# Optimization experiments

Measured on AMD Instinct MI355X. Metric: run time of the kernel, lower is better.

## Reference

```python
import jax, jax.numpy as jnp
import numpy as np

B, N, S, K = 8, 4096, 1024, 128   # clouds, pts/cloud, fps samples (ratio=0.25), max neighbors
R = 0.2                            # radius
DIN = 3                            # point feature dim


def setup_inputs() -> dict:
    key = jax.random.key(0)
    ks = jax.random.split(key, 8)
    x = jax.random.normal(ks[0], (B * N, DIN), dtype=jnp.float32)
    pos = jax.random.uniform(ks[1], (B * N, 3), dtype=jnp.float32)
    batch = jnp.repeat(jnp.arange(B, dtype=jnp.int32), N)
    def lin(k, fi, fo):
        return jax.random.normal(k, (fi, fo), dtype=jnp.float32) / np.float32(np.sqrt(fi))
    W1 = lin(ks[2], DIN + 3, 64); b1 = jnp.zeros((64,), jnp.float32)
    W2 = lin(ks[3], 64, 64);      b2 = jnp.zeros((64,), jnp.float32)
    W3 = lin(ks[4], 64, 128);     b3 = jnp.zeros((128,), jnp.float32)
    return {"x": x, "pos": pos, "W1": W1, "b1": b1, "W2": W2, "b2": b2,
            "W3": W3, "b3": b3, "batch": batch}


def _fps(pos3):
    """Farthest point sampling per cloud. pos3: [B,N,3] -> idx [B,S] (start at point 0)."""
    d0 = jnp.sum((pos3 - pos3[:, :1]) ** 2, axis=-1)  # [B,N]
    def step(min_d, _):
        nxt = jnp.argmax(min_d, axis=1).astype(jnp.int32)             # [B]
        p = jnp.take_along_axis(pos3, nxt[:, None, None], axis=1)      # [B,1,3]
        d = jnp.sum((pos3 - p) ** 2, axis=-1)
        return jnp.minimum(min_d, d), nxt
    _, idxs = jax.lax.scan(step, d0, None, length=S - 1)               # [S-1,B]
    first = jnp.zeros((B, 1), jnp.int32)
    return jnp.concatenate([first, idxs.T], axis=1)                    # [B,S]


def reference(x, pos, W1, b1, W2, b2, W3, b3, batch):
    x3 = x.reshape(B, N, DIN)
    pos3 = pos.reshape(B, N, 3)
    batch2 = batch.reshape(B, N)

    idx = _fps(pos3)                                                   # [B,S]
    q = jnp.take_along_axis(pos3, idx[:, :, None], axis=1)             # [B,S,3]

    # radius ball query, capped at K nearest within R (deterministic variant of torch radius)
    d2 = jnp.sum((q[:, :, None, :] - pos3[:, None, :, :]) ** 2, -1)    # [B,S,N]
    masked = jnp.where(d2 <= R * R, d2, jnp.inf)
    negd, nbr = jax.lax.top_k(-masked, K)                              # [B,S,K]
    valid = jnp.isfinite(negd)                                         # [B,S,K]

    gather = jax.vmap(lambda a, i: a[i])                                # per-cloud fancy gather
    xj = gather(x3, nbr)                                               # [B,S,K,DIN]
    pj = gather(pos3, nbr)                                             # [B,S,K,3]
    rel = pj - q[:, :, None, :]
    feat = jnp.concatenate([xj, rel], axis=-1)                         # [B,S,K,6]

    h = jax.nn.relu(feat @ W1 + b1)
    h = jax.nn.relu(h @ W2 + b2)
    h = h @ W3 + b3                                                    # plain last layer

    h = jnp.where(valid[..., None], h, -jnp.inf)
    out = jnp.max(h, axis=2)                                           # max aggregation [B,S,128]
    out = jnp.where(jnp.any(valid, axis=2)[..., None], out, 0.0)

    x_out = out.reshape(B * S, -1)
    pos_out = q.reshape(B * S, 3)
    batch_out = jnp.take_along_axis(batch2, idx, axis=1).reshape(B * S)
    return x_out, pos_out, batch_out
```

## Files before the change

### kernel.cpp

```cpp
#include <hip/hip_runtime.h>
#include <hip/hip_fp16.h>

#define BB    8
#define NPTS  4096
#define SS    1024
#define KK    128
#define CAP   512
#define NW    248
#define TPB   256
#define PPT   16

typedef _Float16 half8 __attribute__((ext_vector_type(8)));
typedef float    f32x4 __attribute__((ext_vector_type(4)));


struct __align__(16) FpsSm {
    float4 Pl[NPTS];
    unsigned long long wkey[2][4];
};
struct __align__(16) WkSm {
    float cd2[4][CAP];
    int   cidx[4][CAP];
    int   nbrL[4][KK];
    _Float16 W2t[64 * 64];
    _Float16 W3t[128 * 64];
    _Float16 h2buf[4][32 * 64];
    float csh[64];
    float cpart[4][128];
    float b2s[64];
    float b3s[128];
    unsigned tick;
};
union __align__(16) SMem {
    FpsSm f;
    WkSm  w;
    char  pad[84 * 1024];
};

__device__ __forceinline__ void st_rel(unsigned* p, unsigned v) {
    __hip_atomic_store(p, v, __ATOMIC_RELEASE, __HIP_MEMORY_SCOPE_AGENT);
}
__device__ __forceinline__ unsigned ld_acq(unsigned* p) {
    return __hip_atomic_load(p, __ATOMIC_ACQUIRE, __HIP_MEMORY_SCOPE_AGENT);
}

#define DPP_FMAX(CTRL)                                                                  \
    {                                                                                   \
        unsigned o = (unsigned)__builtin_amdgcn_update_dpp(                             \
            (int)__float_as_uint(m), (int)__float_as_uint(m), CTRL, 0xF, 0xF, false);   \
        m = fmaxf(m, __uint_as_float(o));                                               \
    }

__global__ __launch_bounds__(TPB) void fused_kernel(const float* __restrict__ pos,
                                                    const int* __restrict__ batch,
                                                    const float* __restrict__ x,
                                                    const float* __restrict__ W1,
                                                    const float* __restrict__ b1,
                                                    const float* __restrict__ W2,
                                                    const float* __restrict__ b2,
                                                    const float* __restrict__ W3,
                                                    const float* __restrict__ b3,
                                                    float* __restrict__ E,
                                                    float* __restrict__ pos_out,
                                                    float* __restrict__ batch_out,
                                                    float* __restrict__ xout,
                                                    unsigned* __restrict__ sync) {
    __shared__ SMem sm;
    int t = threadIdx.x, w = t >> 6, l = t & 63;

    if (blockIdx.x < BB) {
        __builtin_amdgcn_s_setprio(3);
        int b = blockIdx.x;
        const float* P = pos + (size_t)b * NPTS * 3;

        for (int i = t; i < NPTS; i += TPB) {
            sm.f.Pl[i] = make_float4(P[i * 3 + 0], P[i * 3 + 1], P[i * 3 + 2], 0.f);
        }
        float bval = (float)batch[(size_t)b * NPTS];
        for (int i = t; i < SS; i += TPB) batch_out[b * SS + i] = bval;

        float px[PPT], py[PPT], pz[PPT], md[PPT];
        int base = t * PPT;
#pragma unroll
        for (int j = 0; j < PPT; j++) {
            px[j] = P[(base + j) * 3 + 0];
            py[j] = P[(base + j) * 3 + 1];
            pz[j] = P[(base + j) * 3 + 2];
        }
        float c0x = P[0], c0y = P[1], c0z = P[2];
        float lm = -1.f;
#pragma unroll
        for (int j = 0; j < PPT; j++) {
            float dx = __fsub_rn(px[j], c0x);
            float dy = __fsub_rn(py[j], c0y);
            float dz = __fsub_rn(pz[j], c0z);
            md[j] = __fadd_rn(__fadd_rn(__fmul_rn(dx, dx), __fmul_rn(dy, dy)), __fmul_rn(dz, dz));
            lm = fmaxf(lm, md[j]);
        }
        if (t == 0) {
            float* qp = pos_out + (size_t)(b * SS) * 3;
            qp[0] = c0x; qp[1] = c0y; qp[2] = c0z;
        }
        __syncthreads();

        for (int s = 1; s < SS; s++) {
            int jsel = 0x7FFFFFFF;
#pragma unroll
            for (int j = PPT - 1; j >= 0; j--)
                if (md[j] == lm) jsel = base + j;

            float m = lm;
            DPP_FMAX(0x111)
            DPP_FMAX(0x112)
            DPP_FMAX(0x114)
            DPP_FMAX(0x118)
            DPP_FMAX(0x142)
            DPP_FMAX(0x143)
            float wm = __uint_as_float((unsigned)__builtin_amdgcn_readlane(__float_as_uint(m), 63));

            unsigned long long mask = __ballot(lm == wm);
            int L = __ffsll((long long)mask) - 1;
            int si = __builtin_amdgcn_readlane(jsel, L);

            if (l == 0)
                sm.f.wkey[s & 1][w] = (((unsigned long long)__float_as_uint(wm)) << 32) | (~(unsigned)si);
            __syncthreads();

            const unsigned long long* wk = sm.f.wkey[s & 1];
            unsigned long long g0 = wk[0] > wk[1] ? wk[0] : wk[1];
            unsigned long long g1 = wk[2] > wk[3] ? wk[2] : wk[3];
            unsigned long long g = g0 > g1 ? g0 : g1;
            int gi = (int)(~(unsigned)g);

            float4 c = sm.f.Pl[gi];
            if (t == 0) {
                float* qp = pos_out + (size_t)(b * SS + s) * 3;
                qp[0] = c.x; qp[1] = c.y; qp[2] = c.z;
                if ((s & 63) == 63) st_rel(&sync[b * 32], (unsigned)(s + 1));
            }
#pragma unroll
            for (int j = 0; j < PPT; j++) {
                float dx = __fsub_rn(px[j], c.x);
                float dy = __fsub_rn(py[j], c.y);
                float dz = __fsub_rn(pz[j], c.z);
                float d2 = __fadd_rn(__fadd_rn(__fmul_rn(dx, dx), __fmul_rn(dy, dy)), __fmul_rn(dz, dz));
                md[j] = fminf(md[j], d2);
                lm = (j == 0) ? fmaxf(-1.f, md[0]) : fmaxf(lm, md[j]);
            }
        }
        return;
    }

    int wid = blockIdx.x - BB;
    unsigned* ectr = &sync[256];
    unsigned* qctr = &sync[260];

    for (int id = wid * TPB + t; id < 32768 * 64; id += NW * TPB) {
        int c = id & 63;
        int n = id >> 6;
        float x0 = x[n * 3 + 0], x1 = x[n * 3 + 1], x2 = x[n * 3 + 2];
        float p0 = pos[n * 3 + 0], p1 = pos[n * 3 + 1], p2 = pos[n * 3 + 2];
        float v = x0 * W1[0 * 64 + c] + x1 * W1[1 * 64 + c] + x2 * W1[2 * 64 + c]
                + p0 * W1[3 * 64 + c] + p1 * W1[4 * 64 + c] + p2 * W1[5 * 64 + c];
        E[(size_t)n * 64 + c] = v;
    }
    if (l == 0) __hip_atomic_fetch_add(ectr, 1u, __ATOMIC_RELEASE, __HIP_MEMORY_SCOPE_AGENT);

    for (int i = t; i < 64 * 64; i += TPB) {
        int n = i >> 6, k = i & 63;
        sm.w.W2t[(n << 6) | (k ^ ((n & 7) << 3))] = (_Float16)W2[k * 64 + n];
    }
    for (int i = t; i < 128 * 64; i += TPB) {
        int n = i >> 6, k = i & 63;
        sm.w.W3t[(n << 6) | (k ^ ((n & 7) << 3))] = (_Float16)W3[k * 128 + n];
    }
    if (t < 64) sm.w.b2s[t] = b2[t];
    if (t < 128) sm.w.b3s[t] = b3[t];

    if (t == 0) {
        while (ld_acq(ectr) < NW * 4u) __builtin_amdgcn_s_sleep(16);
    }
    __syncthreads();

    int lhi = l >> 4, llo = l & 15;

    while (true) {
        if (t == 0) {
            unsigned k = __hip_atomic_fetch_add(qctr, 1u, __ATOMIC_RELAXED, __HIP_MEMORY_SCOPE_AGENT);
            sm.w.tick = k;
        }
        __syncthreads();
        unsigned k = sm.w.tick;
        if (k >= 2048u) break;
        int posi = (int)(k >> 3);
        int cb   = (int)(k & 7u);
        int q0g = cb * SS + posi * 4;
        unsigned need = (unsigned)(posi * 4 + 4);
        if (t == 0) {
            while (ld_acq(&sync[cb * 32]) < need) __builtin_amdgcn_s_sleep(16);
        }
        __syncthreads();

        {
            int qi = q0g + w;
            int bBase = cb * NPTS;
            const float* P = pos + (size_t)bBase * 3;
            float qx = pos_out[qi * 3 + 0], qy = pos_out[qi * 3 + 1], qz = pos_out[qi * 3 + 2];

            int total = 0;
            for (int n0 = 0; n0 < NPTS; n0 += 64) {
                int n = n0 + l;
                float xx = P[n * 3 + 0], yy = P[n * 3 + 1], zz = P[n * 3 + 2];
                float dx = __fsub_rn(qx, xx);
                float dy = __fsub_rn(qy, yy);
                float dz = __fsub_rn(qz, zz);
                float d2 = __fadd_rn(__fadd_rn(__fmul_rn(dx, dx), __fmul_rn(dy, dy)), __fmul_rn(dz, dz));
                bool in = (d2 <= 0.04f);
                unsigned long long mask = __ballot(in);
                int mypos = total + (int)__popcll(mask & ((1ull << l) - 1ull));
                if (in && mypos < CAP) { sm.w.cd2[w][mypos] = d2; sm.w.cidx[w][mypos] = n; }
                total += (int)__popcll(mask);
            }

            if (total <= KK) {
                for (int i = l; i < KK; i += 64)
                    sm.w.nbrL[w][i] = bBase + sm.w.cidx[w][i < total ? i : 0];
            } else {
                int nc = total < CAP ? total : CAP;
                unsigned long long key[8];
#pragma unroll
                for (int i = 0; i < 8; i++) {
                    int p = l + (i << 6);
                    key[i] = (p < nc)
                           ? ((((unsigned long long)__float_as_uint(sm.w.cd2[w][p])) << 12) | (unsigned)sm.w.cidx[w][p])
                           : ~0ull;
                }
                unsigned long long lo = 0, hi = ((unsigned long long)0x3D23D70Bu) << 12;
                while (lo < hi) {
                    unsigned long long mid = (lo + hi) >> 1;
                    int cnt = 0;
#pragma unroll
                    for (int i = 0; i < 8; i++) cnt += (int)__popcll(__ballot(key[i] <= mid));
                    if (cnt >= KK) hi = mid; else lo = mid + 1;
                }
                int done = 0;
#pragma unroll
                for (int i = 0; i < 8; i++) {
                    bool s2 = (key[i] <= lo);
                    unsigned long long mk = __ballot(s2);
                    int p2 = done + (int)__popcll(mk & ((1ull << l) - 1ull));
                    if (s2) sm.w.nbrL[w][p2] = bBase + (int)(key[i] & 0xFFFull);
                    done += (int)__popcll(mk);
                }
            }
        }
        __syncthreads();

        for (int qq = 0; qq < 4; qq++) {
            int qi = q0g + qq;
            if (t < 64) {
                float qx = pos_out[qi * 3 + 0], qy = pos_out[qi * 3 + 1], qz = pos_out[qi * 3 + 2];
                sm.w.csh[t] = b1[t] - (qx * W1[3 * 64 + t] + qy * W1[4 * 64 + t] + qz * W1[5 * 64 + t]);
            }
            __syncthreads();

            half8 a2[2][2];
            int row0 = w * 32;
#pragma unroll
            for (int mt = 0; mt < 2; mt++) {
                int r = row0 + mt * 16 + llo;
                int nb = sm.w.nbrL[qq][r];
                const float* Er = E + (size_t)nb * 64;
#pragma unroll
                for (int ks = 0; ks < 2; ks++) {
                    int k0 = lhi * 8 + ks * 32;
                    f32x4 e0 = *(const f32x4*)(Er + k0);
                    f32x4 e1 = *(const f32x4*)(Er + k0 + 4);
                    f32x4 c0 = *(const f32x4*)(sm.w.csh + k0);
                    f32x4 c1 = *(const f32x4*)(sm.w.csh + k0 + 4);
                    half8 a;
#pragma unroll
                    for (int e = 0; e < 4; e++) {
                        a[e]     = (_Float16)fmaxf(e0[e] + c0[e], 0.f);
                        a[4 + e] = (_Float16)fmaxf(e1[e] + c1[e], 0.f);
                    }
                    a2[mt][ks] = a;
                }
            }

            f32x4 acc2[2][4];
#pragma unroll
            for (int mt = 0; mt < 2; mt++)
#pragma unroll
                for (int nt = 0; nt < 4; nt++) acc2[mt][nt] = (f32x4){0.f, 0.f, 0.f, 0.f};
#pragma unroll
            for (int ks = 0; ks < 2; ks++) {
                int k0 = lhi * 8 + ks * 32;
#pragma unroll
                for (int nt = 0; nt < 4; nt++) {
                    int n = nt * 16 + llo;
                    half8 bf = *(const half8*)&sm.w.W2t[(n << 6) | (k0 ^ ((n & 7) << 3))];
#pragma unroll
                    for (int mt = 0; mt < 2; mt++)
                        acc2[mt][nt] = __builtin_amdgcn_mfma_f32_16x16x32_f16(a2[mt][ks], bf, acc2[mt][nt], 0, 0, 0);
                }
            }

            _Float16* hb = sm.w.h2buf[w];
#pragma unroll
            for (int mt = 0; mt < 2; mt++)
#pragma unroll
                for (int nt = 0; nt < 4; nt++)
#pragma unroll
                    for (int r = 0; r < 4; r++) {
                        int lr = mt * 16 + lhi * 4 + r;
                        int n = nt * 16 + llo;
                        float v = fmaxf(acc2[mt][nt][r] + sm.w.b2s[n], 0.f);
                        hb[(lr << 6) | (n ^ ((lr & 7) << 3))] = (_Float16)v;
                    }

            half8 a3[2][2];
#pragma unroll
            for (int mt = 0; mt < 2; mt++)
#pragma unroll
                for (int ks = 0; ks < 2; ks++) {
                    int lr = mt * 16 + llo;
                    int k0 = lhi * 8 + ks * 32;
                    a3[mt][ks] = *(const half8*)&hb[(lr << 6) | (k0 ^ ((lr & 7) << 3))];
                }
            f32x4 acc3[2][8];
#pragma unroll
            for (int mt = 0; mt < 2; mt++)
#pragma unroll
                for (int nt = 0; nt < 8; nt++) acc3[mt][nt] = (f32x4){0.f, 0.f, 0.f, 0.f};
#pragma unroll
            for (int ks = 0; ks < 2; ks++) {
                int k0 = lhi * 8 + ks * 32;
#pragma unroll
                for (int nt = 0; nt < 8; nt++) {
                    int n = nt * 16 + llo;
                    half8 bf = *(const half8*)&sm.w.W3t[(n << 6) | (k0 ^ ((n & 7) << 3))];
#pragma unroll
                    for (int mt = 0; mt < 2; mt++)
                        acc3[mt][nt] = __builtin_amdgcn_mfma_f32_16x16x32_f16(a3[mt][ks], bf, acc3[mt][nt], 0, 0, 0);
                }
            }

#pragma unroll
            for (int nt = 0; nt < 8; nt++) {
                float m = acc3[0][nt][0];
#pragma unroll
                for (int r = 1; r < 4; r++) m = fmaxf(m, acc3[0][nt][r]);
#pragma unroll
                for (int r = 0; r < 4; r++) m = fmaxf(m, acc3[1][nt][r]);
                m = fmaxf(m, __shfl_xor(m, 16));
                m = fmaxf(m, __shfl_xor(m, 32));
                if (l < 16) sm.w.cpart[w][nt * 16 + l] = m;
            }
            __syncthreads();
            if (t < 128) {
                float v = fmaxf(fmaxf(sm.w.cpart[0][t], sm.w.cpart[1][t]),
                                fmaxf(sm.w.cpart[2][t], sm.w.cpart[3][t])) + sm.w.b3s[t];
                xout[(size_t)qi * 128 + t] = v;
            }
            __syncthreads();
        }
        __syncthreads();
    }
}

extern "C" void kernel_launch(void* const* d_in, const int* in_sizes, int n_in,
                              void* d_out, int out_size, void* d_ws, size_t ws_size,
                              hipStream_t stream) {
    const float* x   = (const float*)d_in[0];
    const float* pos = (const float*)d_in[1];
    const float* W1  = (const float*)d_in[2];
    const float* b1  = (const float*)d_in[3];
    const float* W2  = (const float*)d_in[4];
    const float* b2  = (const float*)d_in[5];
    const float* W3  = (const float*)d_in[6];
    const float* b3  = (const float*)d_in[7];
    const int* batch = (const int*)d_in[8];

    float* xout      = (float*)d_out;
    float* pos_out   = xout + (size_t)BB * SS * 128;
    float* batch_out = pos_out + (size_t)BB * SS * 3;

    float* E = (float*)d_ws;
    unsigned* sync = (unsigned*)((char*)d_ws + (size_t)32768 * 64 * 4);
    (void)hipMemsetAsync(sync, 0, 4096, stream);

    fused_kernel<<<dim3(BB + NW), dim3(TPB), 0, stream>>>(
        pos, batch, x, W1, b1, W2, b2, W3, b3, E, pos_out, batch_out, xout, sync);
}
```

Baseline: 619.2 us.

## Process one query per work item and split ball query across warps

The work unit shrinks from four queries to one, and the FPS producer now publishes progress every 16 samples instead of every 64. Workers can therefore start sooner behind the sequential FPS and overlap with it more tightly. The radius scan for a single query is split across the four wavefronts, each covering 1024 points, and the candidate lists are merged through per-wave counts. In exchange, the shared work counter is hit four times as often, there are more block barriers per query, and each wave's candidate cap now applies to a quarter of the cloud, which changes when truncation happens.

```diff
diff --git a/kernel.cpp b/kernel.cpp
--- a/kernel.cpp
+++ b/kernel.cpp
@@ -21,7 +21,8 @@
 struct __align__(16) WkSm {
     float cd2[4][CAP];
     int   cidx[4][CAP];
-    int   nbrL[4][KK];
+    int   nbrL[KK];
+    int   wtot[4];
     _Float16 W2t[64 * 64];
     _Float16 W3t[128 * 64];
     _Float16 h2buf[4][32 * 64];
@@ -136,7 +137,7 @@
             if (t == 0) {
                 float* qp = pos_out + (size_t)(b * SS + s) * 3;
                 qp[0] = c.x; qp[1] = c.y; qp[2] = c.z;
-                if ((s & 63) == 63) st_rel(&sync[b * 32], (unsigned)(s + 1));
+                if ((s & 15) == 15) st_rel(&sync[b * 32], (unsigned)(s + 1));
             }
 #pragma unroll
             for (int j = 0; j < PPT; j++) {
@@ -191,25 +192,29 @@
         }
         __syncthreads();
         unsigned k = sm.w.tick;
-        if (k >= 2048u) break;
+        if (k >= 8192u) break;
         int posi = (int)(k >> 3);
         int cb   = (int)(k & 7u);
-        int q0g = cb * SS + posi * 4;
-        unsigned need = (unsigned)(posi * 4 + 4);
+        int qi = cb * SS + posi;
+        unsigned need = (unsigned)(posi + 1);
         if (t == 0) {
             while (ld_acq(&sync[cb * 32]) < need) __builtin_amdgcn_s_sleep(16);
         }
         __syncthreads();
 
+        int bBase = cb * NPTS;
+        float qx = pos_out[qi * 3 + 0], qy = pos_out[qi * 3 + 1], qz = pos_out[qi * 3 + 2];
+
+        if (t < 64) {
+            sm.w.csh[t] = b1[t] - (qx * W1[3 * 64 + t] + qy * W1[4 * 64 + t] + qz * W1[5 * 64 + t]);
+        }
+
         {
-            int qi = q0g + w;
-            int bBase = cb * NPTS;
             const float* P = pos + (size_t)bBase * 3;
-            float qx = pos_out[qi * 3 + 0], qy = pos_out[qi * 3 + 1], qz = pos_out[qi * 3 + 2];
-
-            int total = 0;
-            for (int n0 = 0; n0 < NPTS; n0 += 64) {
-                int n = n0 + l;
+            int myTotal = 0;
+            int nbase = w * 1024;
+            for (int n0 = 0; n0 < 1024; n0 += 64) {
+                int n = nbase + n0 + l;
                 float xx = P[n * 3 + 0], yy = P[n * 3 + 1], zz = P[n * 3 + 2];
                 float dx = __fsub_rn(qx, xx);
                 float dy = __fsub_rn(qy, yy);
@@ -217,23 +222,41 @@
                 float d2 = __fadd_rn(__fadd_rn(__fmul_rn(dx, dx), __fmul_rn(dy, dy)), __fmul_rn(dz, dz));
                 bool in = (d2 <= 0.04f);
                 unsigned long long mask = __ballot(in);
-                int mypos = total + (int)__popcll(mask & ((1ull << l) - 1ull));
+                int mypos = myTotal + (int)__popcll(mask & ((1ull << l) - 1ull));
                 if (in && mypos < CAP) { sm.w.cd2[w][mypos] = d2; sm.w.cidx[w][mypos] = n; }
-                total += (int)__popcll(mask);
-            }
+                myTotal += (int)__popcll(mask);
+            }
+            if (l == 0) sm.w.wtot[w] = myTotal < CAP ? myTotal : CAP;
+        }
+        __syncthreads();
+
+        {
+            int c0 = sm.w.wtot[0], c1 = sm.w.wtot[1], c2 = sm.w.wtot[2], c3 = sm.w.wtot[3];
+            int off1 = c0, off2 = c0 + c1, off3 = c0 + c1 + c2;
+            int total = off3 + c3;
 
             if (total <= KK) {
-                for (int i = l; i < KK; i += 64)
-                    sm.w.nbrL[w][i] = bBase + sm.w.cidx[w][i < total ? i : 0];
+                for (int i = t; i < KK; i += TPB) {
+                    int p = i < total ? i : 0;
+                    int seg = (p >= off1) + (p >= off2) + (p >= off3);
+                    int sb = seg == 0 ? 0 : (seg == 1 ? off1 : (seg == 2 ? off2 : off3));
+                    sm.w.nbrL[i] = bBase + sm.w.cidx[seg][p - sb];
+                }
             } else {
-                int nc = total < CAP ? total : CAP;
+                int nc = total;
                 unsigned long long key[8];
 #pragma unroll
                 for (int i = 0; i < 8; i++) {
                     int p = l + (i << 6);
-                    key[i] = (p < nc)
-                           ? ((((unsigned long long)__float_as_uint(sm.w.cd2[w][p])) << 12) | (unsigned)sm.w.cidx[w][p])
-                           : ~0ull;
+                    if (p < nc) {
+                        int seg = (p >= off1) + (p >= off2) + (p >= off3);
+                        int sb = seg == 0 ? 0 : (seg == 1 ? off1 : (seg == 2 ? off2 : off3));
+                        int lc = p - sb;
+                        key[i] = (((unsigned long long)__float_as_uint(sm.w.cd2[seg][lc])) << 12)
+                               | (unsigned)sm.w.cidx[seg][lc];
+                    } else {
+                        key[i] = ~0ull;
+                    }
                 }
                 unsigned long long lo = 0, hi = ((unsigned long long)0x3D23D70Bu) << 12;
                 while (lo < hi) {
@@ -249,27 +272,20 @@
                     bool s2 = (key[i] <= lo);
                     unsigned long long mk = __ballot(s2);
                     int p2 = done + (int)__popcll(mk & ((1ull << l) - 1ull));
-                    if (s2) sm.w.nbrL[w][p2] = bBase + (int)(key[i] & 0xFFFull);
+                    if (s2) sm.w.nbrL[p2] = bBase + (int)(key[i] & 0xFFFull);
                     done += (int)__popcll(mk);
                 }
             }
         }
         __syncthreads();
 
-        for (int qq = 0; qq < 4; qq++) {
-            int qi = q0g + qq;
-            if (t < 64) {
-                float qx = pos_out[qi * 3 + 0], qy = pos_out[qi * 3 + 1], qz = pos_out[qi * 3 + 2];
-                sm.w.csh[t] = b1[t] - (qx * W1[3 * 64 + t] + qy * W1[4 * 64 + t] + qz * W1[5 * 64 + t]);
-            }
-            __syncthreads();
-
+        {
             half8 a2[2][2];
             int row0 = w * 32;
 #pragma unroll
             for (int mt = 0; mt < 2; mt++) {
                 int r = row0 + mt * 16 + llo;
-                int nb = sm.w.nbrL[qq][r];
+                int nb = sm.w.nbrL[r];
                 const float* Er = E + (size_t)nb * 64;
 #pragma unroll
                 for (int ks = 0; ks < 2; ks++) {
@@ -365,7 +381,6 @@
             }
             __syncthreads();
         }
-        __syncthreads();
     }
 }
 
```

Measured after the change: 640.3 us. 3.4% more time.
